# Performance work log

Hardware: AMD Instinct MI355X
Metric: run time of the kernel (lower is better)

The kernel has to match this reference:

```python
import math
import jax, jax.numpy as jnp
from jax import lax
import numpy as np

B = 2048
C = 32000
TAU = math.log(32000.0)
LAM = 1.0
BATCH_SIZE = 2048.0
TEMP = 4.0


def lambertw(y, iters=8):
    """Principal-branch Lambert W for real y >= -1/e via Halley iterations."""
    # branch-point expansion init for small y, asymptotic log init for large y
    ey1 = jnp.maximum(jnp.e * y + 1.0, 0.0)
    w_small = -1.0 + jnp.sqrt(2.0 * ey1)
    ys = jnp.maximum(y, 1.0 + 1e-6)
    w_big = jnp.log(ys) - jnp.log(jnp.maximum(jnp.log(ys), 1e-6))
    w = jnp.where(y < 1.0, w_small, w_big)
    for _ in range(iters):
        ew = jnp.exp(w)
        f = w * ew - y
        wp1 = w + 1.0
        denom = ew * wp1 - (w + 2.0) * f / (2.0 * jnp.where(jnp.abs(wp1) > 1e-6, wp1, 1e-6))
        denom = jnp.where(jnp.abs(denom) > 1e-12, denom, 1e-12)
        w = w - f / denom
    return w


def _per_sample_loss(logits, teacher_outputs, targets, ones):
    # cross entropy per sample
    logp = jax.nn.log_softmax(logits, axis=-1)  # [B, C]
    ce = -jnp.take_along_axis(logp, targets[:, None], axis=1)[:, 0]  # [B]
    # temperature-scaled KL(teacher || student), summed over classes
    logp_T = jax.nn.log_softmax(logits / TEMP, axis=-1)
    p_t = jax.nn.softmax(teacher_outputs / TEMP, axis=-1)
    kl = jnp.sum(p_t * (jnp.log(p_t) - logp_T), axis=-1)  # [B]
    return ones[:, 0] * ce + TEMP * TEMP * ones[:, 1] * kl  # [B]


def reference(logits, teacher_outputs, targets, ones):
    base = _per_sample_loss(logits, teacher_outputs, targets, ones)  # [B]
    # sigma computed from detached loss (torch .detach() + cpu numpy round-trip)
    l_i = lax.stop_gradient(base)
    y = 0.5 * jnp.maximum(-2.0 / jnp.e, (l_i - TAU) / LAM)
    sigma = jnp.exp(-lambertw(y))  # [B], no gradient flows through
    loss = (base - TAU) * sigma + LAM * jnp.log(sigma) ** 2
    return loss.sum() / BATCH_SIZE


def setup_inputs() -> dict:
    key = jax.random.key(0)
    k1, k2, k3 = jax.random.split(key, 3)
    return {
        "logits": jax.random.normal(k1, (B, C), dtype=jnp.float32),
        "teacher_outputs": jax.random.normal(k2, (B, C), dtype=jnp.float32),
        "targets": jax.random.randint(k3, (B,), 0, C, dtype=jnp.int32),
        "ones": jnp.ones((B, 2), dtype=jnp.float32),
    }
```

## Files before the change

kernel.cpp:

```cpp
#include <hip/hip_runtime.h>
#include <math.h>

#define NCLASS 32000
#define NROWS  2048
#define T1     320
#define NSTEP  25

#define TAU_D 10.373491181781864
#define E_D   2.718281828459045

__device__ __forceinline__ double lambertw_d(double y) {
    double ey1 = fmax(E_D * y + 1.0, 0.0);
    double w_small = -1.0 + sqrt(2.0 * ey1);
    double ys = fmax(y, 1.0 + 1e-6);
    double ly = log(ys);
    double w_big = ly - log(fmax(ly, 1e-6));
    double w = (y < 1.0) ? w_small : w_big;
#pragma unroll
    for (int i = 0; i < 8; ++i) {
        double ew = exp(w);
        double f = w * ew - y;
        double wp1 = w + 1.0;
        double safe_wp1 = (fabs(wp1) > 1e-6) ? wp1 : 1e-6;
        double denom = ew * wp1 - (w + 2.0) * f / (2.0 * safe_wp1);
        if (!(fabs(denom) > 1e-12)) denom = 1e-12;
        w = w - f / denom;
    }
    return w;
}

__device__ __forceinline__ void upd(float x, float t,
                                    float& s1, float& sT, float& st,
                                    float& A, float& Bv) {
    float ex4 = __expf(x * 0.25f);
    float ex2 = ex4 * ex4;
    s1 += ex2 * ex2;
    sT += ex4;
    float et = __expf(t * 0.25f);
    st += et;
    A  = fmaf(et, t, A);
    Bv = fmaf(et, x, Bv);
}

__global__ __launch_bounds__(T1, 8) void sums_kernel(
    const float* __restrict__ logits,
    const float* __restrict__ teacher,
    float* __restrict__ ws)
{
    const int row = blockIdx.x;
    const size_t base = (size_t)row * NCLASS;
    const float4* __restrict__ lg = (const float4*)(logits  + base);
    const float4* __restrict__ tc = (const float4*)(teacher + base);
    const int tid = threadIdx.x;

    float s1 = 0.f, sT = 0.f, st = 0.f, A = 0.f, Bv = 0.f;

    int j = tid + (row % NSTEP) * T1;

#pragma unroll
    for (int s = 0; s < NSTEP; ++s) {
        const float4 x = lg[j];
        const float4 t = tc[j];
        upd(x.x, t.x, s1, sT, st, A, Bv);
        upd(x.y, t.y, s1, sT, st, A, Bv);
        upd(x.z, t.z, s1, sT, st, A, Bv);
        upd(x.w, t.w, s1, sT, st, A, Bv);
        j += T1;
        if (j >= NSTEP * T1) j -= NSTEP * T1;
    }

#pragma unroll
    for (int off = 32; off > 0; off >>= 1) {
        s1 += __shfl_down(s1, off);
        sT += __shfl_down(sT, off);
        st += __shfl_down(st, off);
        A  += __shfl_down(A,  off);
        Bv += __shfl_down(Bv, off);
    }

    __shared__ float red[T1 / 64][5];
    const int wave = tid >> 6;
    const int lane = tid & 63;
    if (lane == 0) {
        red[wave][0] = s1; red[wave][1] = sT; red[wave][2] = st;
        red[wave][3] = A;  red[wave][4] = Bv;
    }
    __syncthreads();

    if (tid < 5) {
        float acc = 0.f;
#pragma unroll
        for (int w = 0; w < T1 / 64; ++w) acc += red[w][tid];
        ws[row * 5 + tid] = acc;
    }
}

__global__ __launch_bounds__(256) void finalize_kernel(
    const float* __restrict__ logits,
    const int*   __restrict__ targets,
    const float* __restrict__ ones,
    const float* __restrict__ ws,
    float* __restrict__ out)
{
    const int r = blockIdx.x * 256 + threadIdx.x;

    const float fs1 = ws[r * 5 + 0];
    const float fsT = ws[r * 5 + 1];
    const float fst = ws[r * 5 + 2];
    const float fA  = ws[r * 5 + 3];
    const float fB  = ws[r * 5 + 4];

    const float xt = logits[(size_t)r * NCLASS + (size_t)targets[r]];
    const float o0 = ones[2 * r + 0];
    const float o1 = ones[2 * r + 1];

    const double lse   = log((double)fs1);
    const double lseT  = log((double)fsT);
    const double lseTt = log((double)fst);

    const double ce = lse - (double)xt;
    const double kl = ((double)fA - (double)fB) / ((double)fst * 4.0)
                      - lseTt + lseT;

    const double base = (double)o0 * ce + 16.0 * (double)o1 * kl;

    const double y = 0.5 * fmax(-2.0 / E_D, (base - TAU_D));
    const double w = lambertw_d(y);
    const double sigma = exp(-w);
    double loss = (base - TAU_D) * sigma + w * w;

#pragma unroll
    for (int off = 32; off > 0; off >>= 1)
        loss += __shfl_down(loss, off);

    __shared__ double red2[4];
    const int wave = threadIdx.x >> 6;
    const int lane = threadIdx.x & 63;
    if (lane == 0) red2[wave] = loss;
    __syncthreads();

    if (threadIdx.x == 0) {
        double acc = red2[0] + red2[1] + red2[2] + red2[3];
        atomicAdd(out, (float)(acc / 2048.0));
    }
}

extern "C" void kernel_launch(void* const* d_in, const int* in_sizes, int n_in,
                              void* d_out, int out_size, void* d_ws, size_t ws_size,
                              hipStream_t stream) {
    const float* logits  = (const float*)d_in[0];
    const float* teacher = (const float*)d_in[1];
    const int*   targets = (const int*)d_in[2];
    const float* ones    = (const float*)d_in[3];
    float* out = (float*)d_out;
    float* ws  = (float*)d_ws;

    hipMemsetAsync(out, 0, sizeof(float) * (size_t)out_size, stream);

    sums_kernel<<<NROWS, T1, 0, stream>>>(logits, teacher, ws);
    finalize_kernel<<<NROWS / 256, 256, 0, stream>>>(logits, targets, ones, ws, out);
}
```

Before: 506.9 us.

## Stream row tiles through LDS with async global_load_lds four-deep pipeline

Replaces direct float4 register loads in the row-sum kernel with asynchronous global-to-LDS loads into a four-slot shared buffer. Explicit vmcnt waits keep up to three stages in flight while the current one is consumed. Occupancy hint drops from 8 to 4 blocks per CU to fit the added shared memory. It also removes the per-row rotated start offset, so all rows begin at the same column. Each thread reads back only the LDS slot it loaded itself, so no barrier is needed. This relies on hand-counted vmcnt values and adds an LDS round trip, which may or may not beat plain loads for a bandwidth-bound stream.

```diff
diff --git a/kernel.cpp b/kernel.cpp
--- a/kernel.cpp
+++ b/kernel.cpp
@@ -4,10 +4,14 @@
 #define NCLASS 32000
 #define NROWS  2048
 #define T1     320
-#define NSTEP  25
+#define NSTAGE 25
+#define D      4
 
 #define TAU_D 10.373491181781864
 #define E_D   2.718281828459045
+
+#define GAS __attribute__((address_space(1)))
+#define SAS __attribute__((address_space(3)))
 
 __device__ __forceinline__ double lambertw_d(double y) {
     double ey1 = fmax(E_D * y + 1.0, 0.0);
@@ -42,7 +46,7 @@
     Bv = fmaf(et, x, Bv);
 }
 
-__global__ __launch_bounds__(T1, 8) void sums_kernel(
+__global__ __launch_bounds__(T1, 4) void sums_kernel(
     const float* __restrict__ logits,
     const float* __restrict__ teacher,
     float* __restrict__ ws)
@@ -53,20 +57,42 @@
     const float4* __restrict__ tc = (const float4*)(teacher + base);
     const int tid = threadIdx.x;
 
+    __shared__ float4 sb[D][2][T1];
+
     float s1 = 0.f, sT = 0.f, st = 0.f, A = 0.f, Bv = 0.f;
 
-    int j = tid + (row % NSTEP) * T1;
-
-#pragma unroll
-    for (int s = 0; s < NSTEP; ++s) {
-        const float4 x = lg[j];
-        const float4 t = tc[j];
+    auto dma = [&](int slot, int s) {
+        const int j = tid + s * T1;
+        __builtin_amdgcn_global_load_lds(
+            (const GAS unsigned int*)(lg + j),
+            (SAS unsigned int*)&sb[slot][0][tid], 16, 0, 0);
+        __builtin_amdgcn_global_load_lds(
+            (const GAS unsigned int*)(tc + j),
+            (SAS unsigned int*)&sb[slot][1][tid], 16, 0, 0);
+    };
+    auto consume = [&](int slot) {
+        const float4 x = sb[slot][0][tid];
+        const float4 t = sb[slot][1][tid];
         upd(x.x, t.x, s1, sT, st, A, Bv);
         upd(x.y, t.y, s1, sT, st, A, Bv);
         upd(x.z, t.z, s1, sT, st, A, Bv);
         upd(x.w, t.w, s1, sT, st, A, Bv);
-        j += T1;
-        if (j >= NSTEP * T1) j -= NSTEP * T1;
+    };
+
+    dma(0, 0); dma(1, 1); dma(2, 2); dma(3, 3);
+
+#pragma unroll
+    for (int s = 0; s < NSTAGE; ++s) {
+        if (s < NSTAGE - 3)       asm volatile("s_waitcnt vmcnt(6)" ::: "memory");
+        else if (s == NSTAGE - 3) asm volatile("s_waitcnt vmcnt(4)" ::: "memory");
+        else if (s == NSTAGE - 2) asm volatile("s_waitcnt vmcnt(2)" ::: "memory");
+        else                      asm volatile("s_waitcnt vmcnt(0)" ::: "memory");
+
+        consume(s & (D - 1));
+
+        __builtin_amdgcn_sched_barrier(0);
+
+        if (s + D < NSTAGE) dma(s & (D - 1), s + D);
     }
 
 #pragma unroll
```

Result: no change. 505.4 us (-0.3%).
